# Performance work log

Measured on AMD Instinct MI355X. Metric: run time of the kernel, lower is better.

## Reference

```python
import jax, jax.numpy as jnp
import numpy as np

N, E = 20000, 320000
D_IN, HID, HEADS, OUT = 256, 64, 8, 64
K1 = int(np.ceil(0.75 * N))   # 15000 nodes after pool1
K2 = int(np.ceil(0.75 * K1))  # 11250 nodes after pool2
NEG = -1e30


def setup_inputs():
    key = jax.random.key(0)
    ks = jax.random.split(key, 24)
    s = 0.1
    rn = lambda k, shape: jax.random.normal(k, shape, jnp.float32) * s
    HH = HEADS * HID  # 512
    p = {}
    p["x"] = jax.random.normal(ks[0], (N, D_IN), jnp.float32)
    p["edge_index"] = jax.random.randint(ks[1], (2, E), 0, N, dtype=jnp.int32)
    # gat1: GATv2Conv(D_IN -> HID, heads=HEADS), concat output dim HH
    p["g1_wl"] = rn(ks[2], (D_IN, HH)); p["g1_wr"] = rn(ks[3], (D_IN, HH))
    p["g1_att"] = rn(ks[4], (HEADS, HID)); p["g1_b"] = jnp.zeros((HH,), jnp.float32)
    # pool1 scoring GNN: GATConv(HH -> 1, heads=1) + SelectTopK weight
    p["p1_w"] = rn(ks[5], (HH, 1)); p["p1_asrc"] = rn(ks[6], (1,)); p["p1_adst"] = rn(ks[7], (1,))
    p["p1_b"] = jnp.zeros((1,), jnp.float32); p["p1_sel"] = rn(ks[8], (1,)) + 0.5
    # gat2: GATv2Conv(HH -> HID, heads=1)
    p["g2_wl"] = rn(ks[9], (HH, HID)); p["g2_wr"] = rn(ks[10], (HH, HID))
    p["g2_att"] = rn(ks[11], (1, HID)); p["g2_b"] = jnp.zeros((HID,), jnp.float32)
    # pool2 scoring GNN: GATConv(HID -> 1)
    p["p2_w"] = rn(ks[12], (HID, 1)); p["p2_asrc"] = rn(ks[13], (1,)); p["p2_adst"] = rn(ks[14], (1,))
    p["p2_b"] = jnp.zeros((1,), jnp.float32); p["p2_sel"] = rn(ks[15], (1,)) + 0.5
    # MLP head
    p["l1_w"] = rn(ks[16], (2 * HH, HH)); p["l1_b"] = jnp.zeros((HH,), jnp.float32)
    d2 = OUT * (HEADS // 2); d3 = OUT * (HEADS // 4)
    p["l2_w"] = rn(ks[17], (HH, d2)); p["l2_b"] = jnp.zeros((d2,), jnp.float32)
    p["l3_w"] = rn(ks[18], (d2, d3)); p["l3_b"] = jnp.zeros((d3,), jnp.float32)
    p["l4_w"] = rn(ks[19], (d3, 2)); p["l4_b"] = jnp.zeros((2,), jnp.float32)
    return p


def _seg_softmax(e, dst, valid, n):
    # numerically stable segment softmax over destination nodes; invalid edges -> 0
    e = jnp.where(valid[:, None], e, NEG)
    m = jax.ops.segment_max(e, dst, num_segments=n)
    ex = jnp.exp(e - m[dst])
    ex = jnp.where(valid[:, None], ex, 0.0)
    den = jax.ops.segment_sum(ex, dst, num_segments=n)
    return ex / den[dst]


def gatv2(x, src, dst, valid, wl, wr, att, b):
    # GATv2Conv: score = att . LeakyReLU(Wl x_src + Wr x_dst), segment softmax, concat heads
    n = x.shape[0]
    h, c = att.shape
    xl = (x @ wl).reshape(n, h, c)
    xr = (x @ wr).reshape(n, h, c)
    loop = jnp.arange(n, dtype=src.dtype)  # add_self_loops=True
    s = jnp.concatenate([src, loop]); d = jnp.concatenate([dst, loop])
    v = jnp.concatenate([valid, jnp.ones((n,), bool)])
    m = jax.nn.leaky_relu(xl[s] + xr[d], 0.2)          # [E', H, C]
    e = jnp.einsum("ehc,hc->eh", m, att)               # [E', H]
    a = _seg_softmax(e, d, v, n)
    out = jax.ops.segment_sum(a[..., None] * xl[s], d, num_segments=n)
    return out.reshape(n, h * c) + b


def gat_score(x, src, dst, valid, w, asrc, adst, b):
    # GATConv(in -> 1, heads=1): per-node scalar projection score
    n = x.shape[0]
    xl = x @ w                                          # [n, 1]
    al = (xl * asrc).sum(-1); ar = (xl * adst).sum(-1)  # [n]
    loop = jnp.arange(n, dtype=src.dtype)
    s = jnp.concatenate([src, loop]); d = jnp.concatenate([dst, loop])
    v = jnp.concatenate([valid, jnp.ones((n,), bool)])
    e = jax.nn.leaky_relu(al[s] + ar[d], 0.2)[:, None]
    a = _seg_softmax(e, d, v, n)
    return jax.ops.segment_sum(a * xl[s], d, num_segments=n) + b


def sag_pool(x, src, dst, valid, k, w, asrc, adst, b, sel_w):
    # SAGPooling: GNN score -> tanh -> top-k -> x[perm]*score, edge filtering via mask
    attn = gat_score(x, src, dst, valid, w, asrc, adst, b)           # [n, 1]
    score = jnp.tanh((attn * sel_w).sum(-1) / jnp.linalg.norm(sel_w))  # SelectTopK
    vals, perm = jax.lax.top_k(score, k)
    xp = x[perm] * vals[:, None]
    new_id = jnp.full((x.shape[0],), -1, src.dtype).at[perm].set(jnp.arange(k, dtype=src.dtype))
    s2, d2 = new_id[src], new_id[dst]
    v2 = valid & (s2 >= 0) & (d2 >= 0)
    return xp, jnp.where(v2, s2, 0), jnp.where(v2, d2, 0), v2


def _forward(x, edge_index, g1_wl, g1_wr, g1_att, g1_b, p1_w, p1_asrc, p1_adst, p1_b, p1_sel,
             g2_wl, g2_wr, g2_att, g2_b, p2_w, p2_asrc, p2_adst, p2_b, p2_sel,
             l1_w, l1_b, l2_w, l2_b, l3_w, l3_b, l4_w, l4_b):
    src, dst = edge_index[0], edge_index[1]
    valid = jnp.ones((src.shape[0],), bool)
    h = jax.nn.relu(gatv2(x, src, dst, valid, g1_wl, g1_wr, g1_att, g1_b))
    h, s1, d1, v1 = sag_pool(h, src, dst, valid, K1, p1_w, p1_asrc, p1_adst, p1_b, p1_sel)
    # single graph -> global pools are plain reductions over nodes
    x1 = jnp.concatenate([h.max(0, keepdims=True), h.mean(0, keepdims=True)], axis=1)
    h2 = jax.nn.relu(gatv2(h, s1, d1, v1, g2_wl, g2_wr, g2_att, g2_b))
    h2, _, _, _ = sag_pool(h2, s1, d1, v1, K2, p2_w, p2_asrc, p2_adst, p2_b, p2_sel)
    gmax = jnp.tile(h2.max(0, keepdims=True), (1, HEADS))
    gmean = jnp.tile(h2.mean(0, keepdims=True), (1, HEADS))
    z = x1 + jnp.concatenate([gmax, gmean], axis=1)
    z = jax.nn.relu(z @ l1_w + l1_b)   # dropout is identity at eval
    z = jax.nn.relu(z @ l2_w + l2_b)
    z = jax.nn.relu(z @ l3_w + l3_b)
    logits = z @ l4_w + l4_b
    return logits, jax.nn.softmax(logits, axis=-1)


def reference(x, edge_index, g1_wl, g1_wr, g1_att, g1_b, p1_w, p1_asrc, p1_adst, p1_b, p1_sel,
              g2_wl, g2_wr, g2_att, g2_b, p2_w, p2_asrc, p2_adst, p2_b, p2_sel,
              l1_w, l1_b, l2_w, l2_b, l3_w, l3_b, l4_w, l4_b):
    return _forward(x, edge_index, g1_wl, g1_wr, g1_att, g1_b, p1_w, p1_asrc, p1_adst, p1_b, p1_sel,
                    g2_wl, g2_wr, g2_att, g2_b, p2_w, p2_asrc, p2_adst, p2_b, p2_sel,
                    l1_w, l1_b, l2_w, l2_b, l3_w, l3_b, l4_w, l4_b)
```

## Files before the change

kernel.cpp:

```cpp
#include <hip/hip_runtime.h>
#include <math.h>

#define N_NODES 20000
#define E_EDGES 320000
#define DIN     256
#define HHD     512
#define HIDD    64
#define NHEADS  8
#define K1N     15000
#define K2N     11250

typedef unsigned short u16;
typedef __attribute__((ext_vector_type(8))) short bf16x8;
typedef __attribute__((ext_vector_type(4))) float f32x4;

static inline int cdiv(long long a, long long b) { return (int)((a + b - 1) / b); }

__device__ __forceinline__ void atomicMaxF(float* addr, float val) {
  int* ai = (int*)addr;
  int old = __float_as_int(*addr);
  while (__int_as_float(old) < val) {
    int assumed = old;
    old = atomicCAS(ai, assumed, __float_as_int(val));
    if (old == assumed) break;
  }
}

__device__ __forceinline__ u16 f2bf(float x) {
  unsigned u = __float_as_uint(x);
  return (u16)((u + 0x7FFFu + ((u >> 16) & 1u)) >> 16);
}
__device__ __forceinline__ float bfval(u16 b) { return __uint_as_float(((unsigned)b) << 16); }

__device__ __forceinline__ void unpk8(uint4 u, float* v) {
  v[0] = __uint_as_float(u.x << 16); v[1] = __uint_as_float(u.x & 0xffff0000u);
  v[2] = __uint_as_float(u.y << 16); v[3] = __uint_as_float(u.y & 0xffff0000u);
  v[4] = __uint_as_float(u.z << 16); v[5] = __uint_as_float(u.z & 0xffff0000u);
  v[6] = __uint_as_float(u.w << 16); v[7] = __uint_as_float(u.w & 0xffff0000u);
}

__global__ void init_all(int* deg1, int* rank1, float* pools) {
  int i = blockIdx.x * blockDim.x + threadIdx.x;
  if (i < N_NODES) deg1[i] = 0;
  else if (i < 2 * N_NODES) rank1[i - N_NODES] = 0;
  else {
    int idx = i - 2 * N_NODES;
    if (idx < 1152)
      pools[idx] = (idx < 512 || (idx >= 1024 && idx < 1088)) ? -INFINITY : 0.f;
  }
}

__global__ void conv_fused(const float* __restrict__ A, const int* __restrict__ perm,
                           const float* __restrict__ scalev,
                           u16* __restrict__ ah, u16* __restrict__ al, int M, int K,
                           const float* __restrict__ w1, const float* __restrict__ w2,
                           u16* __restrict__ wh, u16* __restrict__ wl, int ncHalf,
                           int aBlocks) {
  if ((int)blockIdx.x < aBlocks) {
    long long i = (long long)blockIdx.x * blockDim.x + threadIdx.x;
    long long e0 = i * 4;
    if (e0 >= (long long)M * K) return;
    int row = (int)(e0 / K), col = (int)(e0 % K);
    int ar = perm ? perm[row] : row;
    float4 v = *(const float4*)(A + (size_t)ar * K + col);
    if (scalev) { float s = scalev[ar]; v.x *= s; v.y *= s; v.z *= s; v.w *= s; }
    u16 h0 = f2bf(v.x), h1 = f2bf(v.y), h2 = f2bf(v.z), h3 = f2bf(v.w);
    u16 l0 = f2bf(v.x - bfval(h0)), l1 = f2bf(v.y - bfval(h1));
    u16 l2 = f2bf(v.z - bfval(h2)), l3 = f2bf(v.w - bfval(h3));
    uint2 hp, lp;
    hp.x = (unsigned)h0 | ((unsigned)h1 << 16); hp.y = (unsigned)h2 | ((unsigned)h3 << 16);
    lp.x = (unsigned)l0 | ((unsigned)l1 << 16); lp.y = (unsigned)l2 | ((unsigned)l3 << 16);
    *(uint2*)(ah + e0) = hp;
    *(uint2*)(al + e0) = lp;
  } else {
    int i = (blockIdx.x - aBlocks) * blockDim.x + threadIdx.x;
    int NT = 2 * ncHalf;
    if (i >= NT * K) return;
    int n = i % NT, k = i / NT;
    float v = (n < ncHalf) ? w1[(size_t)k * ncHalf + n] : w2[(size_t)k * ncHalf + (n - ncHalf)];
    u16 h = f2bf(v);
    u16 l = f2bf(v - bfval(h));
    wh[(size_t)n * K + k] = h;
    wl[(size_t)n * K + k] = l;
  }
}

template<int BT, bool OUTBF>
__global__ __launch_bounds__(256) void gemm_bf16x3(const u16* __restrict__ ah,
                                                   const u16* __restrict__ al,
                                                   const u16* __restrict__ wh,
                                                   const u16* __restrict__ wl,
                                                   void* __restrict__ c1v,
                                                   void* __restrict__ c2v,
                                                   int M, int K, int ncHalf) {
  constexpr int F = BT / 32;
  __shared__ u16 Ah[BT][40], Al[BT][40], Bh[BT][40], Bl[BT][40];
  int tid = threadIdx.x;
  int lane = tid & 63, wid = tid >> 6;
  int wr = (wid >> 1) * (BT / 2), wc = (wid & 1) * (BT / 2);
  int brow = blockIdx.y * BT, bcol = blockIdx.x * BT;
  int fr = lane & 15, kg = lane >> 4;
  f32x4 acc[F][F];
#pragma unroll
  for (int i = 0; i < F; i++)
#pragma unroll
    for (int j = 0; j < F; j++) acc[i][j] = (f32x4){0.f, 0.f, 0.f, 0.f};

  for (int k0 = 0; k0 < K; k0 += 32) {
    constexpr int ITER = (BT * 32) / (256 * 8);
#pragma unroll
    for (int i = 0; i < ITER; i++) {
      int pos = tid + i * 256;
      int row = pos >> 2;
      int kc = (pos & 3) * 8;
      int gr = brow + row;
      float4 z = make_float4(0.f, 0.f, 0.f, 0.f);
      float4 vah = (gr < M) ? *(const float4*)(ah + (size_t)gr * K + k0 + kc) : z;
      float4 val = (gr < M) ? *(const float4*)(al + (size_t)gr * K + k0 + kc) : z;
      *(float4*)(&Ah[row][kc]) = vah;
      *(float4*)(&Al[row][kc]) = val;
      int gn = bcol + row;
      *(float4*)(&Bh[row][kc]) = *(const float4*)(wh + (size_t)gn * K + k0 + kc);
      *(float4*)(&Bl[row][kc]) = *(const float4*)(wl + (size_t)gn * K + k0 + kc);
    }
    __syncthreads();
    bf16x8 fa_h[F], fa_l[F], fb_h[F], fb_l[F];
#pragma unroll
    for (int t = 0; t < F; t++) {
      fa_h[t] = *(const bf16x8*)(&Ah[wr + t * 16 + fr][kg * 8]);
      fa_l[t] = *(const bf16x8*)(&Al[wr + t * 16 + fr][kg * 8]);
      fb_h[t] = *(const bf16x8*)(&Bh[wc + t * 16 + fr][kg * 8]);
      fb_l[t] = *(const bf16x8*)(&Bl[wc + t * 16 + fr][kg * 8]);
    }
#pragma unroll
    for (int i = 0; i < F; i++)
#pragma unroll
      for (int j = 0; j < F; j++) {
        acc[i][j] = __builtin_amdgcn_mfma_f32_16x16x32_bf16(fa_h[i], fb_h[j], acc[i][j], 0, 0, 0);
        acc[i][j] = __builtin_amdgcn_mfma_f32_16x16x32_bf16(fa_h[i], fb_l[j], acc[i][j], 0, 0, 0);
        acc[i][j] = __builtin_amdgcn_mfma_f32_16x16x32_bf16(fa_l[i], fb_h[j], acc[i][j], 0, 0, 0);
      }
    __syncthreads();
  }
#pragma unroll
  for (int i = 0; i < F; i++) {
    int r0 = brow + wr + i * 16 + kg * 4;
#pragma unroll
    for (int j = 0; j < F; j++) {
      int cg = bcol + wc + j * 16 + fr;
      bool first = (cg < ncHalf);
      int cc = first ? cg : cg - ncHalf;
#pragma unroll
      for (int r = 0; r < 4; r++) {
        int gr = r0 + r;
        if (gr < M) {
          if (OUTBF) {
            u16* cp = first ? (u16*)c1v : (u16*)c2v;
            cp[(size_t)gr * ncHalf + cc] = f2bf(acc[i][j][r]);
          } else {
            float* cp = first ? (float*)c1v : (float*)c2v;
            cp[(size_t)gr * ncHalf + cc] = acc[i][j][r];
          }
        }
      }
    }
  }
}

__global__ void deg_count(const int* __restrict__ src, const int* __restrict__ dst,
                          const int* __restrict__ newid, int* __restrict__ deg,
                          int nloops) {
  int i = blockIdx.x * blockDim.x + threadIdx.x;
  if (i >= E_EDGES + nloops) return;
  int d;
  if (i < E_EDGES) {
    if (newid) {
      int s = newid[src[i]]; d = newid[dst[i]];
      if (s < 0 || d < 0) return;
    } else d = dst[i];
  } else d = i - E_EDGES;
  atomicAdd(&deg[d], 1);
}

__global__ __launch_bounds__(1024) void scan_excl(const int* deg, int* rowptr,
                                                  int* cursor, int n) {
  __shared__ int wsum[16];
  __shared__ int carry;
  int tid = threadIdx.x, lane = tid & 63, wid = tid >> 6;
  if (tid == 0) { carry = 0; rowptr[0] = 0; }
  __syncthreads();
  for (int base = 0; base < n; base += 1024) {
    int v = (base + tid < n) ? deg[base + tid] : 0;
    int s = v;
#pragma unroll
    for (int off = 1; off < 64; off <<= 1) {
      int t = __shfl_up(s, off);
      if (lane >= off) s += t;
    }
    if (lane == 63) wsum[wid] = s;
    __syncthreads();
    if (wid == 0) {
      int w = (lane < 16) ? wsum[lane] : 0;
#pragma unroll
      for (int off = 1; off < 16; off <<= 1) {
        int t = __shfl_up(w, off);
        if (lane >= off) w += t;
      }
      if (lane < 16) wsum[lane] = w;
    }
    __syncthreads();
    int incl = s + (wid > 0 ? wsum[wid - 1] : 0) + carry;
    if (base + tid < n) { rowptr[base + tid + 1] = incl; cursor[base + tid] = incl - v; }
    __syncthreads();
    if (tid == 1023) carry = incl;
    __syncthreads();
  }
}

__global__ void csr_scatter(const int* __restrict__ src, const int* __restrict__ dst,
                            const int* __restrict__ newid, int* __restrict__ cursor,
                            int* __restrict__ csr_s, int nloops) {
  int i = blockIdx.x * blockDim.x + threadIdx.x;
  if (i >= E_EDGES + nloops) return;
  int s, d;
  if (i < E_EDGES) {
    s = src[i]; d = dst[i];
    if (newid) {
      s = newid[s]; d = newid[d];
      if (s < 0 || d < 0) return;
    }
  } else s = d = i - E_EDGES;
  int pos = atomicAdd(&cursor[d], 1);
  csr_s[pos] = s;
}

__global__ __launch_bounds__(256) void gat1_fused(const int* __restrict__ rowptr,
                                                  const int* __restrict__ csr_s,
                                                  const u16* __restrict__ xlb,
                                                  const u16* __restrict__ xrb,
                                                  const float* __restrict__ att,
                                                  const float* __restrict__ bias,
                                                  const float* __restrict__ pw,
                                                  float* __restrict__ out,
                                                  float* __restrict__ xls) {
  int lane = threadIdx.x & 63;
  long long t = (long long)blockIdx.x * blockDim.x + threadIdx.x;
  int d = (int)(t >> 6);
  if (d >= N_NODES) return;
  int base = lane * 8;
  float4 a0 = *(const float4*)(att + base);
  float4 a1 = *(const float4*)(att + base + 4);
  float r[8];
  unpk8(*(const uint4*)(xrb + (size_t)d * HHD + base), r);
  float m = -INFINITY, den = 0.f;
  float acc[8] = {0.f, 0.f, 0.f, 0.f, 0.f, 0.f, 0.f, 0.f};
  int b0 = rowptr[d];
  int cnt = rowptr[d + 1] - b0;
  const int* sp = csr_s + b0;

  auto online = [&](uint4 u) {
    float v[8];
    unpk8(u, v);
    float p, tv;
    tv = v[0] + r[0]; tv = tv > 0.f ? tv : 0.2f * tv; p  = tv * a0.x;
    tv = v[1] + r[1]; tv = tv > 0.f ? tv : 0.2f * tv; p += tv * a0.y;
    tv = v[2] + r[2]; tv = tv > 0.f ? tv : 0.2f * tv; p += tv * a0.z;
    tv = v[3] + r[3]; tv = tv > 0.f ? tv : 0.2f * tv; p += tv * a0.w;
    tv = v[4] + r[4]; tv = tv > 0.f ? tv : 0.2f * tv; p += tv * a1.x;
    tv = v[5] + r[5]; tv = tv > 0.f ? tv : 0.2f * tv; p += tv * a1.y;
    tv = v[6] + r[6]; tv = tv > 0.f ? tv : 0.2f * tv; p += tv * a1.z;
    tv = v[7] + r[7]; tv = tv > 0.f ? tv : 0.2f * tv; p += tv * a1.w;
    p += __shfl_xor(p, 1); p += __shfl_xor(p, 2); p += __shfl_xor(p, 4);
    float nm = fmaxf(m, p);
    float w  = __expf(p - nm);
    float sc = __expf(m - nm);
    den = den * sc + w;
#pragma unroll
    for (int k = 0; k < 8; k++) acc[k] = acc[k] * sc + w * v[k];
    m = nm;
  };

  uint4 zz = make_uint4(0u, 0u, 0u, 0u);
  uint4 A = *(const uint4*)(xlb + (size_t)sp[0] * HHD + base);
  uint4 B = (cnt > 1) ? *(const uint4*)(xlb + (size_t)sp[1] * HHD + base) : zz;
  uint4 C = (cnt > 2) ? *(const uint4*)(xlb + (size_t)sp[2] * HHD + base) : zz;
  uint4 D = (cnt > 3) ? *(const uint4*)(xlb + (size_t)sp[3] * HHD + base) : zz;
  int j = 0;
  for (; j + 4 <= cnt; j += 4) {
    uint4 u = A;
    if (j + 4 < cnt) A = *(const uint4*)(xlb + (size_t)sp[j + 4] * HHD + base);
    online(u);
    u = B;
    if (j + 5 < cnt) B = *(const uint4*)(xlb + (size_t)sp[j + 5] * HHD + base);
    online(u);
    u = C;
    if (j + 6 < cnt) C = *(const uint4*)(xlb + (size_t)sp[j + 6] * HHD + base);
    online(u);
    u = D;
    if (j + 7 < cnt) D = *(const uint4*)(xlb + (size_t)sp[j + 7] * HHD + base);
    online(u);
  }
  if (j < cnt) {
    online(A);
    if (j + 1 < cnt) {
      online(B);
      if (j + 2 < cnt) online(C);
    }
  }

  float inv = 1.f / den;
  float4 b0v = *(const float4*)(bias + base);
  float4 b1v = *(const float4*)(bias + base + 4);
  float o[8];
  o[0] = acc[0] * inv + b0v.x; o[1] = acc[1] * inv + b0v.y;
  o[2] = acc[2] * inv + b0v.z; o[3] = acc[3] * inv + b0v.w;
  o[4] = acc[4] * inv + b1v.x; o[5] = acc[5] * inv + b1v.y;
  o[6] = acc[6] * inv + b1v.z; o[7] = acc[7] * inv + b1v.w;
#pragma unroll
  for (int k = 0; k < 8; k++) o[k] = o[k] > 0.f ? o[k] : 0.f;
  float* op = out + (size_t)d * HHD + base;
  *(float4*)(op)     = make_float4(o[0], o[1], o[2], o[3]);
  *(float4*)(op + 4) = make_float4(o[4], o[5], o[6], o[7]);
  float4 w0 = *(const float4*)(pw + base);
  float4 w1 = *(const float4*)(pw + base + 4);
  float sdot = o[0]*w0.x + o[1]*w0.y + o[2]*w0.z + o[3]*w0.w
             + o[4]*w1.x + o[5]*w1.y + o[6]*w1.z + o[7]*w1.w;
#pragma unroll
  for (int off = 32; off > 0; off >>= 1) sdot += __shfl_xor(sdot, off);
  if (lane == 0) xls[d] = sdot;
}

__global__ __launch_bounds__(256) void gat2_fused(const int* __restrict__ rowptr,
                                                  const int* __restrict__ csr_s,
                                                  const float* __restrict__ xl,
                                                  const float* __restrict__ xr,
                                                  const float* __restrict__ att,
                                                  const float* __restrict__ bias,
                                                  const float* __restrict__ pw,
                                                  float* __restrict__ out,
                                                  float* __restrict__ xls, int n) {
  int lane = threadIdx.x & 63;
  int grp = lane >> 4, li = lane & 15;
  long long t = (long long)blockIdx.x * blockDim.x + threadIdx.x;
  int wv = (int)(t >> 6);
  int d = wv * 4 + grp;
  if (d >= n) return;
  int c0 = li * 4;
  float4 av = *(const float4*)(att + c0);
  float4 rv = *(const float4*)(xr + (size_t)d * HIDD + c0);
  float m = -INFINITY, den = 0.f;
  float4 acc = make_float4(0.f, 0.f, 0.f, 0.f);
  int b0 = rowptr[d];
  int cnt = rowptr[d + 1] - b0;
  const int* sp = csr_s + b0;

  auto online = [&](float4 v) {
    float p, tv;
    tv = v.x + rv.x; tv = tv > 0.f ? tv : 0.2f * tv; p  = tv * av.x;
    tv = v.y + rv.y; tv = tv > 0.f ? tv : 0.2f * tv; p += tv * av.y;
    tv = v.z + rv.z; tv = tv > 0.f ? tv : 0.2f * tv; p += tv * av.z;
    tv = v.w + rv.w; tv = tv > 0.f ? tv : 0.2f * tv; p += tv * av.w;
    p += __shfl_xor(p, 1); p += __shfl_xor(p, 2); p += __shfl_xor(p, 4); p += __shfl_xor(p, 8);
    float nm = fmaxf(m, p);
    float w  = __expf(p - nm);
    float sc = __expf(m - nm);
    den = den * sc + w;
    acc.x = acc.x * sc + w * v.x;
    acc.y = acc.y * sc + w * v.y;
    acc.z = acc.z * sc + w * v.z;
    acc.w = acc.w * sc + w * v.w;
    m = nm;
  };

  float4 zz = make_float4(0.f, 0.f, 0.f, 0.f);
  float4 A = *(const float4*)(xl + (size_t)sp[0] * HIDD + c0);
  float4 B = (cnt > 1) ? *(const float4*)(xl + (size_t)sp[1] * HIDD + c0) : zz;
  int j = 0;
  for (; j + 2 <= cnt; j += 2) {
    float4 v = A;
    if (j + 2 < cnt) A = *(const float4*)(xl + (size_t)sp[j + 2] * HIDD + c0);
    online(v);
    v = B;
    if (j + 3 < cnt) B = *(const float4*)(xl + (size_t)sp[j + 3] * HIDD + c0);
    online(v);
  }
  if (j < cnt) online(A);

  float inv = 1.f / den;
  float4 bv = *(const float4*)(bias + c0);
  float4 o;
  o.x = acc.x * inv + bv.x; o.y = acc.y * inv + bv.y;
  o.z = acc.z * inv + bv.z; o.w = acc.w * inv + bv.w;
  o.x = o.x > 0.f ? o.x : 0.f; o.y = o.y > 0.f ? o.y : 0.f;
  o.z = o.z > 0.f ? o.z : 0.f; o.w = o.w > 0.f ? o.w : 0.f;
  *(float4*)(out + (size_t)d * HIDD + c0) = o;
  float4 wv4 = *(const float4*)(pw + c0);
  float sdot = o.x * wv4.x + o.y * wv4.y + o.z * wv4.z + o.w * wv4.w;
  sdot += __shfl_xor(sdot, 1); sdot += __shfl_xor(sdot, 2);
  sdot += __shfl_xor(sdot, 4); sdot += __shfl_xor(sdot, 8);
  if (li == 0) xls[d] = sdot;
}

__global__ __launch_bounds__(256) void pool_score(const int* __restrict__ rowptr,
                                                  const int* __restrict__ csr_s,
                                                  const float* __restrict__ xls,
                                                  const float* __restrict__ asrc,
                                                  const float* __restrict__ adst,
                                                  const float* __restrict__ bias,
                                                  const float* __restrict__ sel,
                                                  float* __restrict__ score, int n) {
  int d = blockIdx.x * blockDim.x + threadIdx.x;
  if (d >= n) return;
  float as = asrc[0], ad = adst[0];
  float ar = xls[d] * ad;
  int b0 = rowptr[d];
  int cnt = rowptr[d + 1] - b0;
  const int* sp = csr_s + b0;
  float m = -INFINITY, den = 0.f, num = 0.f;
  auto upd = [&](float xs) {
    float e = xs * as + ar;
    e = e > 0.f ? e : 0.2f * e;
    float nm = fmaxf(m, e);
    float scv = __expf(m - nm);
    float ex = __expf(e - nm);
    den = den * scv + ex;
    num = num * scv + ex * xs;
    m = nm;
  };
  float xA = xls[sp[0]];
  float xB = (cnt > 1) ? xls[sp[1]] : 0.f;
  float xC = (cnt > 2) ? xls[sp[2]] : 0.f;
  float xD = (cnt > 3) ? xls[sp[3]] : 0.f;
  int j = 0;
  for (; j + 4 <= cnt; j += 4) {
    float x1 = xA;
    if (j + 4 < cnt) xA = xls[sp[j + 4]];
    upd(x1);
    float x2 = xB;
    if (j + 5 < cnt) xB = xls[sp[j + 5]];
    upd(x2);
    float x3 = xC;
    if (j + 6 < cnt) xC = xls[sp[j + 6]];
    upd(x3);
    float x4 = xD;
    if (j + 7 < cnt) xD = xls[sp[j + 7]];
    upd(x4);
  }
  if (j < cnt) {
    upd(xA);
    if (j + 1 < cnt) {
      upd(xB);
      if (j + 2 < cnt) upd(xC);
    }
  }
  float attn = num / den + bias[0];
  float sv = sel[0];
  score[d] = tanhf(attn * sv / fabsf(sv));
}

#define TK_CHUNK 512
__global__ __launch_bounds__(256) void topk_count(const float* __restrict__ score,
                                                  int* __restrict__ rank, int n,
                                                  int* __restrict__ zbuf, int zn) {
  __shared__ float sc[TK_CHUNK];
  if (zbuf) {
    long long fid = ((long long)blockIdx.y * gridDim.x + blockIdx.x) * 256 + threadIdx.x;
    if (fid < zn) zbuf[fid] = 0;
  }
  int i0 = (blockIdx.x * 256 + threadIdx.x) * 4;
  int base = blockIdx.y * TK_CHUNK;
  int cnt = min(TK_CHUNK, n - base);
  for (int j = threadIdx.x; j < cnt; j += 256) sc[j] = score[base + j];
  __syncthreads();
  if (i0 >= n) return;
  int nv = min(4, n - i0);
  float s0 = score[i0];
  float s1 = (nv > 1) ? score[i0 + 1] : 0.f;
  float s2 = (nv > 2) ? score[i0 + 2] : 0.f;
  float s3 = (nv > 3) ? score[i0 + 3] : 0.f;
  int r0 = 0, r1 = 0, r2 = 0, r3 = 0;
  for (int j = 0; j < cnt; j++) {
    float sj = sc[j];
    int gj = base + j;
    r0 += (sj > s0) || ((sj == s0) && (gj < i0));
    r1 += (sj > s1) || ((sj == s1) && (gj < i0 + 1));
    r2 += (sj > s2) || ((sj == s2) && (gj < i0 + 2));
    r3 += (sj > s3) || ((sj == s3) && (gj < i0 + 3));
  }
  if (r0) atomicAdd(&rank[i0], r0);
  if (nv > 1 && r1) atomicAdd(&rank[i0 + 1], r1);
  if (nv > 2 && r2) atomicAdd(&rank[i0 + 2], r2);
  if (nv > 3 && r3) atomicAdd(&rank[i0 + 3], r3);
}

__global__ void topk_assign(const int* __restrict__ rank, int* __restrict__ newid,
                            int* __restrict__ perm, int n, int k) {
  int i = blockIdx.x * blockDim.x + threadIdx.x;
  if (i < n) {
    int r = rank[i];
    newid[i] = (r < k) ? r : -1;
    if (r < k) perm[r] = i;
  }
}

__global__ __launch_bounds__(256) void col_pool_conv(const float* __restrict__ X,
                                                     const int* __restrict__ perm,
                                                     const float* __restrict__ scalev,
                                                     float* __restrict__ omax,
                                                     float* __restrict__ osum,
                                                     u16* __restrict__ ah, u16* __restrict__ al,
                                                     const float* __restrict__ w1,
                                                     const float* __restrict__ w2,
                                                     u16* __restrict__ wh, u16* __restrict__ wl,
                                                     int cpBlocks) {
  int tid = threadIdx.x;
  if ((int)blockIdx.x < cpBlocks) {
    float mx[2] = {-INFINITY, -INFINITY};
    float sm[2] = {0.f, 0.f};
    int rpb = (K1N + cpBlocks - 1) / cpBlocks;
    int rbeg = blockIdx.x * rpb;
    int rend = min(K1N, rbeg + rpb);
    for (int r = rbeg; r < rend; r++) {
      int orow = perm[r];
      float sc = scalev[orow];
      const float* row = X + (size_t)orow * HHD;
#pragma unroll
      for (int sg = 0; sg < 2; sg++) {
        int c = sg * 256 + tid;
        float v = row[c] * sc;
        mx[sg] = fmaxf(mx[sg], v);
        sm[sg] += v;
        u16 h = f2bf(v);
        u16 l = f2bf(v - bfval(h));
        ah[(size_t)r * HHD + c] = h;
        al[(size_t)r * HHD + c] = l;
      }
    }
    if (rbeg < rend) {
#pragma unroll
      for (int sg = 0; sg < 2; sg++) {
        int c = sg * 256 + tid;
        atomicMaxF(&omax[c], mx[sg]);
        atomicAdd(&osum[c], sm[sg]);
      }
    }
  } else {
    int i = (blockIdx.x - cpBlocks) * 256 + tid;
    const int NT = 2 * HIDD;
    if (i >= NT * HHD) return;
    int n = i % NT, k = i / NT;
    float v = (n < HIDD) ? w1[(size_t)k * HIDD + n] : w2[(size_t)k * HIDD + (n - HIDD)];
    u16 h = f2bf(v);
    u16 l = f2bf(v - bfval(h));
    wh[(size_t)n * HHD + k] = h;
    wl[(size_t)n * HHD + k] = l;
  }
}

__global__ __launch_bounds__(256) void col_pool(const float* __restrict__ X,
                                                const int* __restrict__ perm,
                                                const float* __restrict__ scalev,
                                                int rows, int C,
                                                float* __restrict__ omax, float* __restrict__ osum) {
  int tid = threadIdx.x;
  float mx = -INFINITY, sm = 0.f;
  int rpb = (rows + gridDim.x - 1) / gridDim.x;
  int rbeg = blockIdx.x * rpb;
  int rend = min(rows, rbeg + rpb);
  for (int r = rbeg; r < rend; r++) {
    int orow = perm[r];
    float sc = scalev[orow];
    int c = tid;
    if (c < C) {
      float v = X[(size_t)orow * C + c] * sc;
      mx = fmaxf(mx, v);
      sm += v;
    }
  }
  if (rbeg < rend && tid < C) {
    atomicMaxF(&omax[tid], mx);
    atomicAdd(&osum[tid], sm);
  }
}

__global__ __launch_bounds__(256) void mlp_l1(const float* __restrict__ pools,
                                              const float* __restrict__ w1,
                                              const float* __restrict__ b1,
                                              float* __restrict__ z1out) {
  __shared__ float z[1024];
  __shared__ float red[16][17];
  int t = threadIdx.x;
  for (int i = t; i < 1024; i += 256) {
    float xv = (i < 512) ? pools[i] : pools[i] * (1.f / K1N);
    float gv = (i < 512) ? pools[1024 + (i & 63)] : pools[1088 + (i & 63)] * (1.f / K2N);
    z[i] = xv + gv;
  }
  __syncthreads();
  int jl = t & 15, ch = t >> 4;
  int j = blockIdx.x * 16 + jl;
  float p = 0.f;
  for (int k = ch * 64; k < ch * 64 + 64; k++) p += z[k] * w1[(size_t)k * 512 + j];
  red[ch][jl] = p;
  __syncthreads();
  if (t < 16) {
    float s = b1[blockIdx.x * 16 + t];
    for (int c = 0; c < 16; c++) s += red[c][t];
    z1out[blockIdx.x * 16 + t] = s > 0.f ? s : 0.f;
  }
}

__global__ __launch_bounds__(256) void mlp_tail(const float* __restrict__ z1,
                                                const float* __restrict__ w2, const float* __restrict__ b2,
                                                const float* __restrict__ w3, const float* __restrict__ b3,
                                                const float* __restrict__ w4, const float* __restrict__ b4,
                                                float* __restrict__ out) {
  __shared__ float z2[256], z3[128], lg[2];
  int t = threadIdx.x;
  {
    float acc = b2[t];
    for (int k = 0; k < 512; k++) acc += z1[k] * w2[(size_t)k * 256 + t];
    z2[t] = acc > 0.f ? acc : 0.f;
  }
  __syncthreads();
  if (t < 128) {
    float acc = b3[t];
    for (int k = 0; k < 256; k++) acc += z2[k] * w3[(size_t)k * 128 + t];
    z3[t] = acc > 0.f ? acc : 0.f;
  }
  __syncthreads();
  if (t < 2) {
    float acc = b4[t];
    for (int k = 0; k < 128; k++) acc += z3[k] * w4[2 * k + t];
    lg[t] = acc;
  }
  __syncthreads();
  if (t == 0) {
    float m = fmaxf(lg[0], lg[1]);
    float e0 = __expf(lg[0] - m), e1 = __expf(lg[1] - m);
    float s = e0 + e1;
    out[0] = lg[0]; out[1] = lg[1];
    out[2] = e0 / s; out[3] = e1 / s;
  }
}

extern "C" void kernel_launch(void* const* d_in, const int* in_sizes, int n_in,
                              void* d_out, int out_size, void* d_ws, size_t ws_size,
                              hipStream_t stream) {
  const float* x       = (const float*)d_in[0];
  const int*   ei      = (const int*)d_in[1];
  const float* g1_wl   = (const float*)d_in[2];
  const float* g1_wr   = (const float*)d_in[3];
  const float* g1_att  = (const float*)d_in[4];
  const float* g1_b    = (const float*)d_in[5];
  const float* p1_w    = (const float*)d_in[6];
  const float* p1_asrc = (const float*)d_in[7];
  const float* p1_adst = (const float*)d_in[8];
  const float* p1_b    = (const float*)d_in[9];
  const float* p1_sel  = (const float*)d_in[10];
  const float* g2_wl   = (const float*)d_in[11];
  const float* g2_wr   = (const float*)d_in[12];
  const float* g2_att  = (const float*)d_in[13];
  const float* g2_b    = (const float*)d_in[14];
  const float* p2_w    = (const float*)d_in[15];
  const float* p2_asrc = (const float*)d_in[16];
  const float* p2_adst = (const float*)d_in[17];
  const float* p2_b    = (const float*)d_in[18];
  const float* p2_sel  = (const float*)d_in[19];
  const float* l1_w    = (const float*)d_in[20];
  const float* l1_b    = (const float*)d_in[21];
  const float* l2_w    = (const float*)d_in[22];
  const float* l2_b    = (const float*)d_in[23];
  const float* l3_w    = (const float*)d_in[24];
  const float* l3_b    = (const float*)d_in[25];
  const float* l4_w    = (const float*)d_in[26];
  const float* l4_b    = (const float*)d_in[27];

  const int* src = ei;
  const int* dst = ei + E_EDGES;

  if (ws_size < (size_t)33440000 * 4) return;
  float* ws  = (float*)d_ws;
  float* xl1 = ws;
  float* xr1 = ws + 10240000;
  float* h1  = ws + 20480000;
  float* aux = ws + 30720000;

  int*   csr_s1   = (int*)aux;
  int*   rowptr1  = (int*)(aux + 340000);
  int*   deg1     = (int*)(aux + 360064);
  int*   rank1    = (int*)(aux + 380064);
  int*   newid1   = (int*)(aux + 400064);
  float* xls1     = aux + 420064;
  float* scr1     = aux + 440064;
  float* pools    = aux + 460064;
  float* x1max    = pools;
  float* x1sum    = pools + 512;
  float* g2max    = pools + 1024;
  float* g2sum    = pools + 1088;
  int*   perm1    = (int*)(aux + 461248);
  float* z1       = aux + 481248;

  u16* xl1b = (u16*)xl1;
  u16* xr1b = (u16*)xr1;

  u16* ah1 = (u16*)h1;
  u16* al1 = ah1 + 5120000;
  u16* wh1 = al1 + 5120000;
  u16* wl1 = wh1 + 262144;

  u16* ah2 = (u16*)xl1;
  u16* al2 = ah2 + 7680000;
  u16* wh2 = al2 + 7680000;
  u16* wl2 = wh2 + 65536;

  float* a2 = xr1;
  float* xl2      = a2;
  float* xr2      = a2 + 960000;
  float* h2       = a2 + 1920000;
  int*   csr_s2   = (int*)(a2 + 2880000);
  int*   rowptr2  = (int*)(a2 + 3215000);
  int*   deg2     = (int*)(a2 + 3230016);
  int*   rank2    = (int*)(a2 + 3245016);
  int*   newid2   = (int*)(a2 + 3260016);
  float* xls2     = a2 + 3275016;
  float* scr2     = a2 + 3290016;
  int*   perm2    = (int*)(a2 + 3305016);

  dim3 b256(256);
  const int E1 = E_EDGES + N_NODES;
  const int E2 = E_EDGES + K1N;

  init_all<<<cdiv(2 * N_NODES + 1152, 256), b256, 0, stream>>>(deg1, rank1, pools);
  deg_count<<<cdiv(E1, 256), b256, 0, stream>>>(src, dst, nullptr, deg1, N_NODES);
  scan_excl<<<1, 1024, 0, stream>>>(deg1, rowptr1, deg1, N_NODES);
  csr_scatter<<<cdiv(E1, 256), b256, 0, stream>>>(src, dst, nullptr, deg1, csr_s1, N_NODES);

  {
    int aBlocks = cdiv((long long)N_NODES * DIN / 4, 256);
    int wBlocks = cdiv(2 * HHD * DIN, 256);
    conv_fused<<<aBlocks + wBlocks, b256, 0, stream>>>(
        x, nullptr, nullptr, ah1, al1, N_NODES, DIN, g1_wl, g1_wr, wh1, wl1, HHD, aBlocks);
  }
  gemm_bf16x3<128, true><<<dim3(2 * HHD / 128, cdiv(N_NODES, 128)), b256, 0, stream>>>(
      ah1, al1, wh1, wl1, xl1b, xr1b, N_NODES, DIN, HHD);
  gat1_fused<<<cdiv((long long)N_NODES * 64, 256), b256, 0, stream>>>(
      rowptr1, csr_s1, xl1b, xr1b, g1_att, g1_b, p1_w, h1, xls1);

  pool_score<<<cdiv(N_NODES, 256), b256, 0, stream>>>(rowptr1, csr_s1, xls1,
                                                      p1_asrc, p1_adst, p1_b, p1_sel, scr1, N_NODES);
  topk_count<<<dim3(cdiv(N_NODES, 1024), cdiv(N_NODES, TK_CHUNK)), b256, 0, stream>>>(
      scr1, rank1, N_NODES, deg2, 30000);
  topk_assign<<<cdiv(N_NODES, 256), b256, 0, stream>>>(rank1, newid1, perm1, N_NODES, K1N);
  {
    int cpBlocks = 256;
    int wBlocks = cdiv(2 * HIDD * HHD, 256);
    col_pool_conv<<<cpBlocks + wBlocks, b256, 0, stream>>>(
        h1, perm1, scr1, x1max, x1sum, ah2, al2, g2_wl, g2_wr, wh2, wl2, cpBlocks);
  }

  deg_count<<<cdiv(E2, 256), b256, 0, stream>>>(src, dst, newid1, deg2, K1N);
  scan_excl<<<1, 1024, 0, stream>>>(deg2, rowptr2, deg2, K1N);
  csr_scatter<<<cdiv(E2, 256), b256, 0, stream>>>(src, dst, newid1, deg2, csr_s2, K1N);

  gemm_bf16x3<64, false><<<dim3(2 * HIDD / 64, cdiv(K1N, 64)), b256, 0, stream>>>(
      ah2, al2, wh2, wl2, xl2, xr2, K1N, HHD, HIDD);
  gat2_fused<<<cdiv((long long)K1N * 16, 256), b256, 0, stream>>>(
      rowptr2, csr_s2, xl2, xr2, g2_att, g2_b, p2_w, h2, xls2, K1N);

  pool_score<<<cdiv(K1N, 256), b256, 0, stream>>>(rowptr2, csr_s2, xls2,
                                                  p2_asrc, p2_adst, p2_b, p2_sel, scr2, K1N);
  topk_count<<<dim3(cdiv(K1N, 1024), cdiv(K1N, TK_CHUNK)), b256, 0, stream>>>(
      scr2, rank2, K1N, nullptr, 0);
  topk_assign<<<cdiv(K1N, 256), b256, 0, stream>>>(rank2, newid2, perm2, K1N, K2N);
  col_pool<<<128, b256, 0, stream>>>(h2, perm2, scr2, K2N, HIDD, g2max, g2sum);

  mlp_l1<<<32, b256, 0, stream>>>(pools, l1_w, l1_b, z1);
  mlp_tail<<<1, b256, 0, stream>>>(z1, l2_w, l2_b, l3_w, l3_b, l4_w, l4_b, (float*)d_out);
}
```

Baseline: 557.9 us.

## Replace pairwise top-k ranking with single-block radix select, split MLP tail

Swaps the O(n^2) pairwise-comparison top-k (count plus assign kernels, atomics on rank) for a single 1024-thread block that does a three-level radix select on order-preserving float keys, then a block-wide prefix scan to assign new ids and perm. Ties at the threshold are broken by index order, so the selection matches the old ranking. The single-block MLP tail is split into multi-block layer kernels and a small final reduction kernel to spread the matvec work. The trade-off is that top-k now runs on one block only and the MLP adds kernel launches, and the output id order changes from score order to index order.

```diff
diff --git a/kernel.cpp b/kernel.cpp
--- a/kernel.cpp
+++ b/kernel.cpp
@@ -39,12 +39,16 @@
   v[6] = __uint_as_float(u.w << 16); v[7] = __uint_as_float(u.w & 0xffff0000u);
 }
 
-__global__ void init_all(int* deg1, int* rank1, float* pools) {
+__device__ __forceinline__ unsigned fkey(float s) {
+  unsigned b = __float_as_uint(s);
+  return (b & 0x80000000u) ? ~b : (b | 0x80000000u);
+}
+
+__global__ void init_all(int* deg1, float* pools) {
   int i = blockIdx.x * blockDim.x + threadIdx.x;
   if (i < N_NODES) deg1[i] = 0;
-  else if (i < 2 * N_NODES) rank1[i - N_NODES] = 0;
   else {
-    int idx = i - 2 * N_NODES;
+    int idx = i - N_NODES;
     if (idx < 1152)
       pools[idx] = (idx < 512 || (idx >= 1024 && idx < 1088)) ? -INFINITY : 0.f;
   }
@@ -458,48 +462,109 @@
   score[d] = tanhf(attn * sv / fabsf(sv));
 }
 
-#define TK_CHUNK 512
-__global__ __launch_bounds__(256) void topk_count(const float* __restrict__ score,
-                                                  int* __restrict__ rank, int n,
-                                                  int* __restrict__ zbuf, int zn) {
-  __shared__ float sc[TK_CHUNK];
-  if (zbuf) {
-    long long fid = ((long long)blockIdx.y * gridDim.x + blockIdx.x) * 256 + threadIdx.x;
-    if (fid < zn) zbuf[fid] = 0;
-  }
-  int i0 = (blockIdx.x * 256 + threadIdx.x) * 4;
-  int base = blockIdx.y * TK_CHUNK;
-  int cnt = min(TK_CHUNK, n - base);
-  for (int j = threadIdx.x; j < cnt; j += 256) sc[j] = score[base + j];
-  __syncthreads();
-  if (i0 >= n) return;
-  int nv = min(4, n - i0);
-  float s0 = score[i0];
-  float s1 = (nv > 1) ? score[i0 + 1] : 0.f;
-  float s2 = (nv > 2) ? score[i0 + 2] : 0.f;
-  float s3 = (nv > 3) ? score[i0 + 3] : 0.f;
-  int r0 = 0, r1 = 0, r2 = 0, r3 = 0;
-  for (int j = 0; j < cnt; j++) {
-    float sj = sc[j];
-    int gj = base + j;
-    r0 += (sj > s0) || ((sj == s0) && (gj < i0));
-    r1 += (sj > s1) || ((sj == s1) && (gj < i0 + 1));
-    r2 += (sj > s2) || ((sj == s2) && (gj < i0 + 2));
-    r3 += (sj > s3) || ((sj == s3) && (gj < i0 + 3));
-  }
-  if (r0) atomicAdd(&rank[i0], r0);
-  if (nv > 1 && r1) atomicAdd(&rank[i0 + 1], r1);
-  if (nv > 2 && r2) atomicAdd(&rank[i0 + 2], r2);
-  if (nv > 3 && r3) atomicAdd(&rank[i0 + 3], r3);
-}
-
-__global__ void topk_assign(const int* __restrict__ rank, int* __restrict__ newid,
-                            int* __restrict__ perm, int n, int k) {
-  int i = blockIdx.x * blockDim.x + threadIdx.x;
-  if (i < n) {
-    int r = rank[i];
-    newid[i] = (r < k) ? r : -1;
-    if (r < k) perm[r] = i;
+__global__ __launch_bounds__(1024) void tk_topk(const float* __restrict__ score, int n, int k,
+                                                int* __restrict__ newid, int* __restrict__ perm,
+                                                int* __restrict__ zbuf, int zn) {
+  __shared__ unsigned bins[2048];
+  __shared__ unsigned wsum[16];
+  __shared__ unsigned sb[4];
+  int tid = threadIdx.x, lane = tid & 63, wid = tid >> 6;
+
+  for (int i = tid; i < zn; i += 1024) zbuf[i] = 0;
+
+  unsigned pref = 0;
+  unsigned kneed = (unsigned)k;
+
+  for (int level = 0; level < 3; level++) {
+    const int shift = (level == 0) ? 21 : (level == 1) ? 10 : 0;
+    const unsigned mask = (level == 2) ? 1023u : 2047u;
+    for (int b = tid; b < 2048; b += 1024) bins[b] = 0;
+    __syncthreads();
+    for (int i = tid; i < n; i += 1024) {
+      unsigned key = fkey(score[i]);
+      bool match = (level == 0) ? true
+                 : (level == 1) ? ((key >> 21) == pref)
+                                : ((key >> 10) == pref);
+      if (match) atomicAdd(&bins[(key >> shift) & mask], 1u);
+    }
+    __syncthreads();
+    unsigned c0 = bins[2 * tid], c1 = bins[2 * tid + 1];
+    unsigned v = c0 + c1;
+    unsigned s = v;
+#pragma unroll
+    for (int off = 1; off < 64; off <<= 1) {
+      unsigned t2 = __shfl_up(s, off);
+      if (lane >= off) s += t2;
+    }
+    if (lane == 63) wsum[wid] = s;
+    __syncthreads();
+    if (wid == 0) {
+      unsigned w = (lane < 16) ? wsum[lane] : 0;
+#pragma unroll
+      for (int off = 1; off < 16; off <<= 1) {
+        unsigned t2 = __shfl_up(w, off);
+        if (lane >= off) w += t2;
+      }
+      if (lane < 16) wsum[lane] = w;
+    }
+    __syncthreads();
+    unsigned incl = s + (wid > 0 ? wsum[wid - 1] : 0);
+    unsigned excl = incl - v;
+    if (tid == 1023) sb[0] = incl;
+    __syncthreads();
+    unsigned TOT = sb[0];
+    unsigned target = TOT - kneed;
+    unsigned ip0 = excl + c0;
+    unsigned ip1 = ip0 + c1;
+    if (excl <= target && target < ip0) { sb[1] = 2u * tid;     sb[2] = TOT - ip0; }
+    if (ip0  <= target && target < ip1) { sb[1] = 2u * tid + 1; sb[2] = TOT - ip1; }
+    __syncthreads();
+    pref = (pref << ((level == 2) ? 10 : 11)) | sb[1];
+    kneed -= sb[2];
+    __syncthreads();
+  }
+  const unsigned U = pref, rem = kneed;
+
+  unsigned carry = 0;
+  for (int base = 0; base < n; base += 1024) {
+    int i = base + tid;
+    bool valid = i < n;
+    unsigned key = valid ? fkey(score[i]) : 0u;
+    unsigned gt  = (valid && key >  U) ? 1u : 0u;
+    unsigned tie = (valid && key == U) ? 1u : 0u;
+    unsigned v = gt | (tie << 16);
+    unsigned s = v;
+#pragma unroll
+    for (int off = 1; off < 64; off <<= 1) {
+      unsigned t2 = __shfl_up(s, off);
+      if (lane >= off) s += t2;
+    }
+    if (lane == 63) wsum[wid] = s;
+    __syncthreads();
+    if (wid == 0) {
+      unsigned w = (lane < 16) ? wsum[lane] : 0;
+#pragma unroll
+      for (int off = 1; off < 16; off <<= 1) {
+        unsigned t2 = __shfl_up(w, off);
+        if (lane >= off) w += t2;
+      }
+      if (lane < 16) wsum[lane] = w;
+    }
+    __syncthreads();
+    unsigned incl = s + (wid > 0 ? wsum[wid - 1] : 0);
+    unsigned pfx = (incl - v) + carry;
+    unsigned gtpfx = pfx & 0xFFFFu, tiepfx = pfx >> 16;
+    unsigned tsel = (tiepfx < rem) ? tiepfx : rem;
+    bool selq = gt || (tie && tiepfx < rem);
+    unsigned id = gtpfx + tsel;
+    if (valid) {
+      newid[i] = selq ? (int)id : -1;
+      if (selq) perm[id] = i;
+    }
+    if (tid == 1023) sb[0] = incl + carry;
+    __syncthreads();
+    carry = sb[0];
+    __syncthreads();
   }
 }
 
@@ -609,36 +674,48 @@
   }
 }
 
-__global__ __launch_bounds__(256) void mlp_tail(const float* __restrict__ z1,
-                                                const float* __restrict__ w2, const float* __restrict__ b2,
-                                                const float* __restrict__ w3, const float* __restrict__ b3,
-                                                const float* __restrict__ w4, const float* __restrict__ b4,
-                                                float* __restrict__ out) {
-  __shared__ float z2[256], z3[128], lg[2];
+template<int NIN>
+__global__ __launch_bounds__(256) void mlp_layer(const float* __restrict__ in,
+                                                 const float* __restrict__ w,
+                                                 const float* __restrict__ b,
+                                                 float* __restrict__ out, int nout) {
+  __shared__ float red[16][17];
   int t = threadIdx.x;
-  {
-    float acc = b2[t];
-    for (int k = 0; k < 512; k++) acc += z1[k] * w2[(size_t)k * 256 + t];
-    z2[t] = acc > 0.f ? acc : 0.f;
-  }
+  int jl = t & 15, ch = t >> 4;
+  int j = blockIdx.x * 16 + jl;
+  constexpr int CH = NIN / 16;
+  float p = 0.f;
+  for (int k = ch * CH; k < (ch + 1) * CH; k++) p += in[k] * w[(size_t)k * nout + j];
+  red[ch][jl] = p;
   __syncthreads();
-  if (t < 128) {
-    float acc = b3[t];
-    for (int k = 0; k < 256; k++) acc += z2[k] * w3[(size_t)k * 128 + t];
-    z3[t] = acc > 0.f ? acc : 0.f;
-  }
-  __syncthreads();
-  if (t < 2) {
-    float acc = b4[t];
-    for (int k = 0; k < 128; k++) acc += z3[k] * w4[2 * k + t];
-    lg[t] = acc;
-  }
+  if (t < 16) {
+    float s = b[blockIdx.x * 16 + t];
+    for (int c = 0; c < 16; c++) s += red[c][t];
+    out[blockIdx.x * 16 + t] = s > 0.f ? s : 0.f;
+  }
+}
+
+__global__ __launch_bounds__(128) void mlp_final(const float* __restrict__ z3,
+                                                 const float* __restrict__ w4,
+                                                 const float* __restrict__ b4,
+                                                 float* __restrict__ out) {
+  int t = threadIdx.x;
+  float v = z3[t];
+  float p0 = v * w4[2 * t], p1 = v * w4[2 * t + 1];
+#pragma unroll
+  for (int off = 32; off > 0; off >>= 1) {
+    p0 += __shfl_xor(p0, off);
+    p1 += __shfl_xor(p1, off);
+  }
+  __shared__ float s0[2], s1[2];
+  if ((t & 63) == 0) { s0[t >> 6] = p0; s1[t >> 6] = p1; }
   __syncthreads();
   if (t == 0) {
-    float m = fmaxf(lg[0], lg[1]);
-    float e0 = __expf(lg[0] - m), e1 = __expf(lg[1] - m);
+    float l0 = s0[0] + s0[1] + b4[0], l1 = s1[0] + s1[1] + b4[1];
+    float m = fmaxf(l0, l1);
+    float e0 = __expf(l0 - m), e1 = __expf(l1 - m);
     float s = e0 + e1;
-    out[0] = lg[0]; out[1] = lg[1];
+    out[0] = l0; out[1] = l1;
     out[2] = e0 / s; out[3] = e1 / s;
   }
 }
@@ -688,7 +765,6 @@
   int*   csr_s1   = (int*)aux;
   int*   rowptr1  = (int*)(aux + 340000);
   int*   deg1     = (int*)(aux + 360064);
-  int*   rank1    = (int*)(aux + 380064);
   int*   newid1   = (int*)(aux + 400064);
   float* xls1     = aux + 420064;
   float* scr1     = aux + 440064;
@@ -699,6 +775,8 @@
   float* g2sum    = pools + 1088;
   int*   perm1    = (int*)(aux + 461248);
   float* z1       = aux + 481248;
+  float* z2       = aux + 481760;
+  float* z3       = aux + 482016;
 
   u16* xl1b = (u16*)xl1;
   u16* xr1b = (u16*)xr1;
@@ -720,7 +798,6 @@
   int*   csr_s2   = (int*)(a2 + 2880000);
   int*   rowptr2  = (int*)(a2 + 3215000);
   int*   deg2     = (int*)(a2 + 3230016);
-  int*   rank2    = (int*)(a2 + 3245016);
   int*   newid2   = (int*)(a2 + 3260016);
   float* xls2     = a2 + 3275016;
   float* scr2     = a2 + 3290016;
@@ -730,7 +807,7 @@
   const int E1 = E_EDGES + N_NODES;
   const int E2 = E_EDGES + K1N;
 
-  init_all<<<cdiv(2 * N_NODES + 1152, 256), b256, 0, stream>>>(deg1, rank1, pools);
+  init_all<<<cdiv(N_NODES + 1152, 256), b256, 0, stream>>>(deg1, pools);
   deg_count<<<cdiv(E1, 256), b256, 0, stream>>>(src, dst, nullptr, deg1, N_NODES);
   scan_excl<<<1, 1024, 0, stream>>>(deg1, rowptr1, deg1, N_NODES);
   csr_scatter<<<cdiv(E1, 256), b256, 0, stream>>>(src, dst, nullptr, deg1, csr_s1, N_NODES);
@@ -748,9 +825,7 @@
 
   pool_score<<<cdiv(N_NODES, 256), b256, 0, stream>>>(rowptr1, csr_s1, xls1,
                                                       p1_asrc, p1_adst, p1_b, p1_sel, scr1, N_NODES);
-  topk_count<<<dim3(cdiv(N_NODES, 1024), cdiv(N_NODES, TK_CHUNK)), b256, 0, stream>>>(
-      scr1, rank1, N_NODES, deg2, 30000);
-  topk_assign<<<cdiv(N_NODES, 256), b256, 0, stream>>>(rank1, newid1, perm1, N_NODES, K1N);
+  tk_topk<<<1, 1024, 0, stream>>>(scr1, N_NODES, K1N, newid1, perm1, deg2, 15000);
   {
     int cpBlocks = 256;
     int wBlocks = cdiv(2 * HIDD * HHD, 256);
@@ -769,11 +844,11 @@
 
   pool_score<<<cdiv(K1N, 256), b256, 0, stream>>>(rowptr2, csr_s2, xls2,
                                                   p2_asrc, p2_adst, p2_b, p2_sel, scr2, K1N);
-  topk_count<<<dim3(cdiv(K1N, 1024), cdiv(K1N, TK_CHUNK)), b256, 0, stream>>>(
-      scr2, rank2, K1N, nullptr, 0);
-  topk_assign<<<cdiv(K1N, 256), b256, 0, stream>>>(rank2, newid2, perm2, K1N, K2N);
+  tk_topk<<<1, 1024, 0, stream>>>(scr2, K1N, K2N, newid2, perm2, nullptr, 0);
   col_pool<<<128, b256, 0, stream>>>(h2, perm2, scr2, K2N, HIDD, g2max, g2sum);
 
   mlp_l1<<<32, b256, 0, stream>>>(pools, l1_w, l1_b, z1);
-  mlp_tail<<<1, b256, 0, stream>>>(z1, l2_w, l2_b, l3_w, l3_b, l4_w, l4_b, (float*)d_out);
-}
+  mlp_layer<512><<<16, b256, 0, stream>>>(z1, l2_w, l2_b, z2, 256);
+  mlp_layer<256><<<8, b256, 0, stream>>>(z2, l3_w, l3_b, z3, 128);
+  mlp_final<<<1, 128, 0, stream>>>(z3, l4_w, l4_b, (float*)d_out);
+}
```

Measured after the change: 479.0 us. -14.1%, faster.
